# Optimization experiments

Hardware: AMD Instinct MI355X
Metric: run time of the kernel (lower is better)

Reference implementation:

```python
import jax, jax.numpy as jnp
import numpy as np

N_NODES = 50000
N_EDGES = 800000
IN_FEAT = 128
HEADS = 8
HEAD_DIM = 16  # out_feat // num_heads = 128 // 8
NEG_SLOPE = 0.2


def setup_inputs() -> dict:
    key = jax.random.key(0)
    ks = jax.random.split(key, 8)
    g = 1.0 / np.sqrt(IN_FEAT)
    return {
        "x": jax.random.normal(ks[0], (N_NODES, IN_FEAT), jnp.float32),
        "efeat": jax.random.normal(ks[1], (N_EDGES, IN_FEAT), jnp.float32),
        "src": jax.random.randint(ks[2], (N_EDGES,), 0, N_NODES),
        "dst": jax.random.randint(ks[3], (N_EDGES,), 0, N_NODES),
        "W_src": jax.random.normal(ks[4], (HEADS * HEAD_DIM, IN_FEAT), jnp.float32) * g,
        "b_src": jnp.zeros((HEADS * HEAD_DIM,), jnp.float32),
        "W_dst": jax.random.normal(ks[5], (HEADS * HEAD_DIM, IN_FEAT), jnp.float32) * g,
        "b_dst": jnp.zeros((HEADS * HEAD_DIM,), jnp.float32),
        "W_edge": jax.random.normal(ks[6], (HEADS * HEAD_DIM, IN_FEAT), jnp.float32) * g,
        "attn": jax.random.normal(ks[7], (HEADS, HEAD_DIM), jnp.float32) * (1.0 / np.sqrt(HEAD_DIM)),
    }


def reference(x, efeat, src, dst, W_src, b_src, W_dst, b_dst, W_edge, attn):
    H, D = HEADS, HEAD_DIM
    # node/edge projections: [N,H,D] / [E,H,D]
    feat_src = (x @ W_src.T + b_src).reshape(-1, H, D)
    feat_dst = (x @ W_dst.T + b_dst).reshape(-1, H, D)
    feat_edge = (efeat @ W_edge.T).reshape(-1, H, D)

    # per-edge GATv2 score: LeakyReLU(src + dst + edge) . attn  -> [E,H]
    fs = feat_src[src]                                    # gather [E,H,D]
    tmp = fs + feat_dst[dst] + feat_edge
    e = jnp.where(tmp >= 0, tmp, NEG_SLOPE * tmp)
    score = jnp.einsum('ehd,hd->eh', e, attn)

    # edge softmax normalized per destination node
    m = jax.ops.segment_max(score, dst, num_segments=N_NODES)     # [N,H]
    ex = jnp.exp(score - jax.lax.stop_gradient(m)[dst])
    z = jax.ops.segment_sum(ex, dst, num_segments=N_NODES)        # [N,H]
    a = ex / z[dst]                                               # [E,H]

    # weighted scatter-sum of (src + edge) messages
    msg = (fs + feat_edge) * a[:, :, None]                        # [E,H,D]
    h = jax.ops.segment_sum(msg, dst, num_segments=N_NODES)       # [N,H,D]

    # res_fc is None since in_feat == H*D; activation = relu
    h = jax.nn.relu(h)
    return h.reshape(N_NODES, H * D)
```

## Files before the change

kernel.cpp:

```cpp
#include <hip/hip_runtime.h>
#include <hip/hip_bf16.h>

#define NNODES 50000
#define NEDGES 800000
#define NEG_SLOPE 0.2f
#define N_PAD 50176

typedef float f32x4 __attribute__((ext_vector_type(4)));
typedef float f32x2 __attribute__((ext_vector_type(2)));
typedef __bf16 bf16x8 __attribute__((ext_vector_type(8)));
typedef __bf16 bf16x4 __attribute__((ext_vector_type(4)));
typedef __bf16 bf16x2 __attribute__((ext_vector_type(2)));

__global__ __launch_bounds__(256) void convert_w3(
    const float* __restrict__ W0, const float* __restrict__ W1,
    const float* __restrict__ W2, __bf16* __restrict__ out)
{
  int m = blockIdx.x >> 4;
  const float* W = (m == 0) ? W0 : ((m == 1) ? W1 : W2);
  __bf16* o = out + m * 16384;
  int i = (blockIdx.x & 15) * 1024 + threadIdx.x * 4;
  int r = i >> 7, cx = i & 127;
  f32x4 v = *(const f32x4*)(W + i);
  int kb = cx >> 3, ko = cx & 7;
  int off = r * 128 + ((kb ^ (r & 15)) << 3) + ko;
  bf16x4 pk = { (__bf16)v.x, (__bf16)v.y, (__bf16)v.z, (__bf16)v.w };
  *(bf16x4*)(o + off) = pk;
}

template<int OUT_BF16, int HAS_BIAS, int SCATTER>
__global__ __launch_bounds__(256, 2) void gemm_proj(
    const float* __restrict__ A, const __bf16* __restrict__ Wsw,
    const float* __restrict__ bias, const int* __restrict__ rank,
    void* __restrict__ outp, int M)
{
  __shared__ __bf16 sB[128 * 128];
  const int t = threadIdx.x;
  const int m0 = blockIdx.x * 128;

  #pragma unroll
  for (int it = 0; it < 8; ++it) {
    int lin = it * 2048 + t * 8;
    *(bf16x8*)(sB + lin) = *(const bf16x8*)(Wsw + lin);
  }

  const int w = t >> 6, lane = t & 63;
  const int rsel = lane & 15, quad = lane >> 4;

  bf16x8 af[4][2];
  #pragma unroll
  for (int mi = 0; mi < 2; ++mi) {
    int gr = m0 + w * 32 + mi * 16 + rsel;
    #pragma unroll
    for (int kk = 0; kk < 4; ++kk) {
      f32x4 v0 = {0.f, 0.f, 0.f, 0.f}, v1 = {0.f, 0.f, 0.f, 0.f};
      if (gr < M) {
        const float* p = A + (size_t)gr * 128 + kk * 32 + quad * 8;
        v0 = *(const f32x4*)p;
        v1 = *(const f32x4*)(p + 4);
      }
      af[kk][mi] = (bf16x8){ (__bf16)v0.x, (__bf16)v0.y, (__bf16)v0.z, (__bf16)v0.w,
                             (__bf16)v1.x, (__bf16)v1.y, (__bf16)v1.z, (__bf16)v1.w };
    }
  }

  f32x4 acc[2][8];
  f32x4 zero = {0.f, 0.f, 0.f, 0.f};
  #pragma unroll
  for (int mi = 0; mi < 2; ++mi)
    #pragma unroll
    for (int ni = 0; ni < 8; ++ni) acc[mi][ni] = zero;

  __syncthreads();

  #pragma unroll
  for (int kk = 0; kk < 4; ++kk) {
    int kb0 = kk * 4 + quad;
    bf16x8 bfr[8];
    #pragma unroll
    for (int ni = 0; ni < 8; ++ni) {
      int r = ni * 16 + rsel;
      bfr[ni] = *(const bf16x8*)(sB + r * 128 + ((kb0 ^ (r & 15)) << 3));
    }
    #pragma unroll
    for (int mi = 0; mi < 2; ++mi)
      #pragma unroll
      for (int ni = 0; ni < 8; ++ni)
        acc[mi][ni] = __builtin_amdgcn_mfma_f32_16x16x32_bf16(af[kk][mi], bfr[ni], acc[mi][ni], 0, 0, 0);
  }

  int orow[2][4];
  #pragma unroll
  for (int mi = 0; mi < 2; ++mi)
    #pragma unroll
    for (int r4 = 0; r4 < 4; ++r4) {
      int grow = m0 + w * 32 + mi * 16 + quad * 4 + r4;
      orow[mi][r4] = (SCATTER && grow < M) ? rank[grow] : grow;
    }

  #pragma unroll
  for (int mi = 0; mi < 2; ++mi) {
    #pragma unroll
    for (int ni = 0; ni < 8; ++ni) {
      #pragma unroll
      for (int r4 = 0; r4 < 4; ++r4) {
        int grow = m0 + w * 32 + mi * 16 + quad * 4 + r4;
        int col = ni * 16 + rsel;
        if (grow < M) {
          float v = acc[mi][ni][r4];
          if (HAS_BIAS) v += bias[col];
          if (OUT_BF16) ((__bf16*)outp)[(size_t)orow[mi][r4] * 128 + col] = (__bf16)v;
          else          ((float*)outp)[(size_t)orow[mi][r4] * 128 + col] = v;
        }
      }
    }
  }
}

__global__ void hist_kernel(const int* __restrict__ dst, int* __restrict__ deg,
                            int* __restrict__ arr){
  int e = blockIdx.x * 256 + threadIdx.x;
  arr[e] = atomicAdd(&deg[dst[e]], 1);
}

__global__ void scan_local(const int* __restrict__ deg, int* __restrict__ scanned,
                           int* __restrict__ bsum){
  __shared__ int s[1024];
  int t = threadIdx.x, i = blockIdx.x * 1024 + t;
  int v = deg[i];
  s[t] = v; __syncthreads();
  #pragma unroll
  for (int off = 1; off < 1024; off <<= 1){
    int x = (t >= off) ? s[t - off] : 0;
    __syncthreads();
    s[t] += x;
    __syncthreads();
  }
  scanned[i] = s[t] - v;
  if (t == 1023) bsum[blockIdx.x] = s[t];
}

__global__ void scan_sums(int* __restrict__ bsum){
  __shared__ int s[64];
  int t = threadIdx.x;
  int v = (t < 49) ? bsum[t] : 0;
  s[t] = v; __syncthreads();
  #pragma unroll
  for (int off = 1; off < 64; off <<= 1){
    int x = (t >= off) ? s[t - off] : 0;
    __syncthreads();
    s[t] += x;
    __syncthreads();
  }
  bsum[t] = s[t] - v;
}

__global__ void scan_add(const int* __restrict__ scanned, const int* __restrict__ bsum,
                         int* __restrict__ row_start){
  int i = blockIdx.x * 256 + threadIdx.x;
  if (i < N_PAD) row_start[i] = scanned[i] + bsum[i >> 10];
}

__global__ void scatter_kernel(const int* __restrict__ dst, const int* __restrict__ src,
                               const int* __restrict__ row_start, int* __restrict__ rank,
                               int* __restrict__ src_perm){
  int e = blockIdx.x * 256 + threadIdx.x;
  int pos = row_start[dst[e]] + rank[e];
  rank[e] = pos;
  src_perm[pos] = src[e];
}

__global__ __launch_bounds__(256) void aggregate_fused(
    const int* __restrict__ row_start, const int* __restrict__ deg,
    const int* __restrict__ src_perm, const float* __restrict__ fs,
    const float* __restrict__ fd, const __bf16* __restrict__ fe,
    const float* __restrict__ attn, float* __restrict__ out)
{
  int wv = threadIdx.x >> 6, lane = threadIdx.x & 63;
  int n = blockIdx.x * 4 + wv;
  int row = row_start[n], dg = deg[n];
  int c = lane << 1;
  f32x2 fdv = *(const f32x2*)(fd + (size_t)n * 128 + c);
  f32x2 atv = *(const f32x2*)(attn + c);
  float acc0 = 0.f, acc1 = 0.f, zs = 0.f;
  const __bf16* fep = fe + (size_t)row * 128 + c;

  #define EDGE_BODY(FV, EV)                                            \
    {                                                                  \
      float v0 = (FV).x + (float)(EV).x;                               \
      float v1 = (FV).y + (float)(EV).y;                               \
      float t0 = v0 + fdv.x; t0 = t0 >= 0.f ? t0 : NEG_SLOPE * t0;     \
      float t1 = v1 + fdv.y; t1 = t1 >= 0.f ? t1 : NEG_SLOPE * t1;     \
      float p = t0 * atv.x + t1 * atv.y;                               \
      p += __shfl_xor(p, 1);                                           \
      p += __shfl_xor(p, 2);                                           \
      p += __shfl_xor(p, 4);                                           \
      float ex = __expf(p);                                            \
      acc0 += ex * v0; acc1 += ex * v1; zs += ex;                      \
    }

  for (int base = 0; base < dg; base += 64){
    int cnt = min(64, dg - base);
    int si = 0;
    if (lane < cnt) si = src_perm[row + base + lane];
    int j = 0;
    for (; j + 4 <= cnt; j += 4){
      int s0 = __shfl(si, j,     64);
      int s1 = __shfl(si, j + 1, 64);
      int s2 = __shfl(si, j + 2, 64);
      int s3 = __shfl(si, j + 3, 64);
      f32x2 f0 = *(const f32x2*)(fs + (size_t)s0 * 128 + c);
      f32x2 f1 = *(const f32x2*)(fs + (size_t)s1 * 128 + c);
      f32x2 f2 = *(const f32x2*)(fs + (size_t)s2 * 128 + c);
      f32x2 f3 = *(const f32x2*)(fs + (size_t)s3 * 128 + c);
      bf16x2 e0 = *(const bf16x2*)(fep + (size_t)(base + j)     * 128);
      bf16x2 e1 = *(const bf16x2*)(fep + (size_t)(base + j + 1) * 128);
      bf16x2 e2 = *(const bf16x2*)(fep + (size_t)(base + j + 2) * 128);
      bf16x2 e3 = *(const bf16x2*)(fep + (size_t)(base + j + 3) * 128);
      EDGE_BODY(f0, e0)
      EDGE_BODY(f1, e1)
      EDGE_BODY(f2, e2)
      EDGE_BODY(f3, e3)
    }
    for (; j < cnt; ++j){
      int s0 = __shfl(si, j, 64);
      f32x2 f0 = *(const f32x2*)(fs + (size_t)s0 * 128 + c);
      bf16x2 e0 = *(const bf16x2*)(fep + (size_t)(base + j) * 128);
      EDGE_BODY(f0, e0)
    }
  }
  #undef EDGE_BODY

  float rz = zs > 0.f ? 1.f / zs : 0.f;
  float o0 = acc0 * rz, o1 = acc1 * rz;
  f32x2 ov = { o0 > 0.f ? o0 : 0.f, o1 > 0.f ? o1 : 0.f };
  *(f32x2*)(out + (size_t)n * 128 + c) = ov;
}

extern "C" void kernel_launch(void* const* d_in, const int* in_sizes, int n_in,
                              void* d_out, int out_size, void* d_ws, size_t ws_size,
                              hipStream_t stream)
{
  const float* x      = (const float*)d_in[0];
  const float* efeat  = (const float*)d_in[1];
  const int*   src    = (const int*)d_in[2];
  const int*   dst    = (const int*)d_in[3];
  const float* W_src  = (const float*)d_in[4];
  const float* b_src  = (const float*)d_in[5];
  const float* W_dst  = (const float*)d_in[6];
  const float* b_dst  = (const float*)d_in[7];
  const float* W_edge = (const float*)d_in[8];
  const float* attn   = (const float*)d_in[9];

  char* ws = (char*)d_ws;
  float*  feat_src  = (float*)(ws + 0);
  float*  feat_dst  = (float*)(ws + 25600000);
  __bf16* fe        = (__bf16*)(ws + 51200000);
  int*    src_perm  = (int*)  (ws + 256000000);
  int*    rank      = (int*)  (ws + 259200000);
  int*    row_start = (int*)  (ws + 262400000);
  int*    scanned   = (int*)  (ws + 262801408);
  int*    deg       = (int*)  (ws + 263002112);
  int*    bsum      = (int*)  (ws + 263202816);
  __bf16* wsw       = (__bf16*)(ws + 263203840);

  hipMemsetAsync(deg, 0, 200704, stream);

  convert_w3<<<48, 256, 0, stream>>>(W_src, W_dst, W_edge, wsw);

  hist_kernel   <<<3125, 256, 0, stream>>>(dst, deg, rank);
  scan_local    <<<49, 1024, 0, stream>>>(deg, scanned, bsum);
  scan_sums     <<<1, 64, 0, stream>>>(bsum);
  scan_add      <<<196, 256, 0, stream>>>(scanned, bsum, row_start);
  scatter_kernel<<<3125, 256, 0, stream>>>(dst, src, row_start, rank, src_perm);

  gemm_proj<0,1,0><<<391, 256, 0, stream>>>(x, wsw,           b_src, nullptr, feat_src, NNODES);
  gemm_proj<0,1,0><<<391, 256, 0, stream>>>(x, wsw + 16384,   b_dst, nullptr, feat_dst, NNODES);
  gemm_proj<1,0,1><<<6250, 256, 0, stream>>>(efeat, wsw + 32768, nullptr, rank, fe, NEDGES);

  aggregate_fused<<<12500, 256, 0, stream>>>(row_start, deg, src_perm, feat_src,
                                             feat_dst, fe, attn, (float*)d_out);
}
```

Before: 782.4 us.

## Make edge projection GEMM persistent with register prefetch and packed bf16 stores

The projection GEMM becomes a persistent grid-stride loop. The weight tile is loaded into LDS once per block and the next A tile's fp32 rows are prefetched into registers while the current tile runs its MFMAs. The edge GEMM launches 512 blocks over 6250 tiles instead of one block per tile, which amortizes the LDS weight load and overlaps global loads with compute. The bf16 scattered output now pairs adjacent columns via a lane shuffle into 32-bit stores. The cost is more register pressure from the 16 prefetch vectors, which may limit occupancy.

Measured after the change: 935.3 us. 1.2x slower.

```diff
diff --git a/kernel.cpp b/kernel.cpp
--- a/kernel.cpp
+++ b/kernel.cpp
@@ -32,88 +32,123 @@
 __global__ __launch_bounds__(256, 2) void gemm_proj(
     const float* __restrict__ A, const __bf16* __restrict__ Wsw,
     const float* __restrict__ bias, const int* __restrict__ rank,
-    void* __restrict__ outp, int M)
+    void* __restrict__ outp, int M, int ntiles)
 {
   __shared__ __bf16 sB[128 * 128];
   const int t = threadIdx.x;
-  const int m0 = blockIdx.x * 128;
-
   #pragma unroll
   for (int it = 0; it < 8; ++it) {
     int lin = it * 2048 + t * 8;
     *(bf16x8*)(sB + lin) = *(const bf16x8*)(Wsw + lin);
   }
+  __syncthreads();
 
   const int w = t >> 6, lane = t & 63;
   const int rsel = lane & 15, quad = lane >> 4;
-
+  const int rbase = w * 32 + rsel;
+
+  f32x4 raw[16];
   bf16x8 af[4][2];
-  #pragma unroll
-  for (int mi = 0; mi < 2; ++mi) {
-    int gr = m0 + w * 32 + mi * 16 + rsel;
-    #pragma unroll
-    for (int kk = 0; kk < 4; ++kk) {
-      f32x4 v0 = {0.f, 0.f, 0.f, 0.f}, v1 = {0.f, 0.f, 0.f, 0.f};
-      if (gr < M) {
-        const float* p = A + (size_t)gr * 128 + kk * 32 + quad * 8;
-        v0 = *(const f32x4*)p;
-        v1 = *(const f32x4*)(p + 4);
+
+  auto load_tile = [&](int tt) {
+    #pragma unroll
+    for (int mi = 0; mi < 2; ++mi) {
+      int gr = tt * 128 + rbase + mi * 16;
+      const float* p = A + (size_t)gr * 128 + (quad << 3);
+      bool ok = gr < M;
+      #pragma unroll
+      for (int kk = 0; kk < 4; ++kk) {
+        f32x4 z4 = {0.f, 0.f, 0.f, 0.f};
+        raw[mi * 8 + kk * 2]     = ok ? *(const f32x4*)(p + kk * 32)     : z4;
+        raw[mi * 8 + kk * 2 + 1] = ok ? *(const f32x4*)(p + kk * 32 + 4) : z4;
       }
-      af[kk][mi] = (bf16x8){ (__bf16)v0.x, (__bf16)v0.y, (__bf16)v0.z, (__bf16)v0.w,
-                             (__bf16)v1.x, (__bf16)v1.y, (__bf16)v1.z, (__bf16)v1.w };
-    }
-  }
-
-  f32x4 acc[2][8];
-  f32x4 zero = {0.f, 0.f, 0.f, 0.f};
-  #pragma unroll
-  for (int mi = 0; mi < 2; ++mi)
-    #pragma unroll
-    for (int ni = 0; ni < 8; ++ni) acc[mi][ni] = zero;
-
-  __syncthreads();
-
-  #pragma unroll
-  for (int kk = 0; kk < 4; ++kk) {
-    int kb0 = kk * 4 + quad;
-    bf16x8 bfr[8];
-    #pragma unroll
-    for (int ni = 0; ni < 8; ++ni) {
-      int r = ni * 16 + rsel;
-      bfr[ni] = *(const bf16x8*)(sB + r * 128 + ((kb0 ^ (r & 15)) << 3));
-    }
+    }
+  };
+
+  int tile = blockIdx.x;
+  load_tile(tile);
+
+  while (true) {
+    #pragma unroll
+    for (int kk = 0; kk < 4; ++kk)
+      #pragma unroll
+      for (int mi = 0; mi < 2; ++mi) {
+        f32x4 v0 = raw[mi * 8 + kk * 2], v1 = raw[mi * 8 + kk * 2 + 1];
+        af[kk][mi] = (bf16x8){ (__bf16)v0.x, (__bf16)v0.y, (__bf16)v0.z, (__bf16)v0.w,
+                               (__bf16)v1.x, (__bf16)v1.y, (__bf16)v1.z, (__bf16)v1.w };
+      }
+
+    int cur = tile;
+    tile += gridDim.x;
+    if (tile < ntiles) load_tile(tile);
+
+    int m0 = cur * 128;
+    int orow[2][4];
     #pragma unroll
     for (int mi = 0; mi < 2; ++mi)
-      #pragma unroll
-      for (int ni = 0; ni < 8; ++ni)
-        acc[mi][ni] = __builtin_amdgcn_mfma_f32_16x16x32_bf16(af[kk][mi], bfr[ni], acc[mi][ni], 0, 0, 0);
-  }
-
-  int orow[2][4];
-  #pragma unroll
-  for (int mi = 0; mi < 2; ++mi)
-    #pragma unroll
-    for (int r4 = 0; r4 < 4; ++r4) {
-      int grow = m0 + w * 32 + mi * 16 + quad * 4 + r4;
-      orow[mi][r4] = (SCATTER && grow < M) ? rank[grow] : grow;
-    }
-
-  #pragma unroll
-  for (int mi = 0; mi < 2; ++mi) {
-    #pragma unroll
-    for (int ni = 0; ni < 8; ++ni) {
       #pragma unroll
       for (int r4 = 0; r4 < 4; ++r4) {
         int grow = m0 + w * 32 + mi * 16 + quad * 4 + r4;
-        int col = ni * 16 + rsel;
-        if (grow < M) {
-          float v = acc[mi][ni][r4];
-          if (HAS_BIAS) v += bias[col];
-          if (OUT_BF16) ((__bf16*)outp)[(size_t)orow[mi][r4] * 128 + col] = (__bf16)v;
-          else          ((float*)outp)[(size_t)orow[mi][r4] * 128 + col] = v;
+        orow[mi][r4] = (SCATTER && grow < M) ? rank[grow] : grow;
+      }
+
+    f32x4 acc[2][8];
+    f32x4 zero = {0.f, 0.f, 0.f, 0.f};
+    #pragma unroll
+    for (int mi = 0; mi < 2; ++mi)
+      #pragma unroll
+      for (int ni = 0; ni < 8; ++ni) acc[mi][ni] = zero;
+
+    #pragma unroll
+    for (int kk = 0; kk < 4; ++kk) {
+      int kb0 = kk * 4 + quad;
+      bf16x8 bfr[8];
+      #pragma unroll
+      for (int ni = 0; ni < 8; ++ni) {
+        int r = ni * 16 + rsel;
+        bfr[ni] = *(const bf16x8*)(sB + r * 128 + ((kb0 ^ (r & 15)) << 3));
+      }
+      #pragma unroll
+      for (int mi = 0; mi < 2; ++mi)
+        #pragma unroll
+        for (int ni = 0; ni < 8; ++ni)
+          acc[mi][ni] = __builtin_amdgcn_mfma_f32_16x16x32_bf16(af[kk][mi], bfr[ni], acc[mi][ni], 0, 0, 0);
+    }
+
+    if (OUT_BF16) {
+      #pragma unroll
+      for (int mi = 0; mi < 2; ++mi)
+        #pragma unroll
+        for (int r4 = 0; r4 < 4; ++r4) {
+          int grow = m0 + w * 32 + mi * 16 + quad * 4 + r4;
+          #pragma unroll
+          for (int ni = 0; ni < 8; ++ni) {
+            float v = acc[mi][ni][r4];
+            float vx = __shfl_xor(v, 1);
+            if (!(rsel & 1) && grow < M) {
+              bf16x2 pkv = { (__bf16)v, (__bf16)vx };
+              *(bf16x2*)((__bf16*)outp + (size_t)orow[mi][r4] * 128 + ni * 16 + rsel) = pkv;
+            }
+          }
         }
-      }
-    }
+    } else {
+      #pragma unroll
+      for (int mi = 0; mi < 2; ++mi)
+        #pragma unroll
+        for (int ni = 0; ni < 8; ++ni)
+          #pragma unroll
+          for (int r4 = 0; r4 < 4; ++r4) {
+            int grow = m0 + w * 32 + mi * 16 + quad * 4 + r4;
+            int col = ni * 16 + rsel;
+            if (grow < M) {
+              float v = acc[mi][ni][r4];
+              if (HAS_BIAS) v += bias[col];
+              ((float*)outp)[(size_t)orow[mi][r4] * 128 + col] = v;
+            }
+          }
+    }
+
+    if (tile >= ntiles) break;
   }
 }
 
@@ -274,9 +309,9 @@
   scan_add      <<<196, 256, 0, stream>>>(scanned, bsum, row_start);
   scatter_kernel<<<3125, 256, 0, stream>>>(dst, src, row_start, rank, src_perm);
 
-  gemm_proj<0,1,0><<<391, 256, 0, stream>>>(x, wsw,           b_src, nullptr, feat_src, NNODES);
-  gemm_proj<0,1,0><<<391, 256, 0, stream>>>(x, wsw + 16384,   b_dst, nullptr, feat_dst, NNODES);
-  gemm_proj<1,0,1><<<6250, 256, 0, stream>>>(efeat, wsw + 32768, nullptr, rank, fe, NEDGES);
+  gemm_proj<0,1,0><<<391, 256, 0, stream>>>(x, wsw,           b_src, nullptr, feat_src, NNODES, 391);
+  gemm_proj<0,1,0><<<391, 256, 0, stream>>>(x, wsw + 16384,   b_dst, nullptr, feat_dst, NNODES, 391);
+  gemm_proj<1,0,1><<<512, 256, 0, stream>>>(efeat, wsw + 32768, nullptr, rank, fe, NEDGES, 6250);
 
   aggregate_fused<<<12500, 256, 0, stream>>>(row_start, deg, src_perm, feat_src,
                                              feat_dst, fe, attn, (float*)d_out);
```
